# Kernel tuning notes

Measured on AMD Instinct MI355X. Metric: run time of the kernel, lower is better.

Reference implementation:

```python
import jax, jax.numpy as jnp
import numpy as np

B, S, H = 4, 2048, 576
NH, NKV, HD = 9, 3, 64
GROUPS = NH // NKV
ROPE_THETA = 100000.0
MAX_POS = 8192


def _rope_tables():
    inv_freq = 1.0 / (ROPE_THETA ** (jnp.arange(0, HD, 2, dtype=jnp.float32) / HD))
    t = jnp.arange(MAX_POS, dtype=jnp.float32)
    freqs = jnp.outer(t, inv_freq)              # [MAX_POS, HD//2]
    emb = jnp.concatenate([freqs, freqs], axis=-1)  # [MAX_POS, HD]
    return jnp.cos(emb), jnp.sin(emb)


def _rotate_half(x):
    x1, x2 = x[..., : HD // 2], x[..., HD // 2 :]
    return jnp.concatenate([-x2, x1], axis=-1)


def setup_inputs() -> dict:
    key = jax.random.key(0)
    k1, k2, k3, k4, k5 = jax.random.split(key, 5)
    hidden_states = jax.random.normal(k1, (B, S, H), dtype=jnp.float32)
    # causal additive mask [B,1,S,S]: 0 where allowed, large negative above diagonal
    causal = jnp.triu(jnp.ones((S, S), dtype=bool), k=1)
    attention_mask = jnp.where(causal, jnp.float32(-1e9), jnp.float32(0.0))[None, None]
    attention_mask = jnp.broadcast_to(attention_mask, (B, 1, S, S))
    position_ids = jnp.broadcast_to(jnp.arange(S, dtype=jnp.int32)[None, :], (B, S))
    scale = 1.0 / np.sqrt(H)
    Wq = jax.random.normal(k2, (NH * HD, H), dtype=jnp.float32) * scale
    Wk = jax.random.normal(k3, (NKV * HD, H), dtype=jnp.float32) * scale
    Wv = jax.random.normal(k4, (NKV * HD, H), dtype=jnp.float32) * scale
    Wo = jax.random.normal(k5, (H, NH * HD), dtype=jnp.float32) * scale
    return {"hidden_states": hidden_states, "attention_mask": attention_mask,
            "position_ids": position_ids, "Wq": Wq, "Wk": Wk, "Wv": Wv, "Wo": Wo}


def reference(hidden_states, attention_mask, position_ids, Wq, Wk, Wv, Wo):
    bsz, q_len, _ = hidden_states.shape
    cos_cached, sin_cached = _rope_tables()
    # projections (nn.Linear: x @ W.T), reshape to [B, heads, S, HD]
    q = (hidden_states @ Wq.T).reshape(bsz, q_len, NH, HD).transpose(0, 2, 1, 3)
    k = (hidden_states @ Wk.T).reshape(bsz, q_len, NKV, HD).transpose(0, 2, 1, 3)
    v = (hidden_states @ Wv.T).reshape(bsz, q_len, NKV, HD).transpose(0, 2, 1, 3)
    # RoPE: gather cos/sin per position, broadcast over heads
    cos = cos_cached[position_ids][:, None]  # [B,1,S,HD]
    sin = sin_cached[position_ids][:, None]
    q = q * cos + _rotate_half(q) * sin
    k = k * cos + _rotate_half(k) * sin
    # GQA: repeat_interleave kv heads
    k = jnp.repeat(k, GROUPS, axis=1)  # [B,NH,S,HD]
    v = jnp.repeat(v, GROUPS, axis=1)
    scores = jnp.einsum('bhqd,bhkd->bhqk', q, k) / np.sqrt(HD)
    scores = scores + attention_mask
    probs = jax.nn.softmax(scores.astype(jnp.float32), axis=-1).astype(q.dtype)
    attn = jnp.einsum('bhqk,bhkd->bhqd', probs, v)
    attn = attn.transpose(0, 2, 1, 3).reshape(bsz, q_len, NH * HD)
    return attn @ Wo.T
```

## Files before the change

### kernel.cpp

```cpp
#include <hip/hip_runtime.h>
#include <hip/hip_bf16.h>
#include <math.h>

#define Bsz 4
#define Slen 2048
#define Hdim 576
#define NH 9
#define NKV 3
#define HD 64

typedef __bf16 bf16_t;
typedef __bf16 bf16x8 __attribute__((ext_vector_type(8)));
typedef float f32x4 __attribute__((ext_vector_type(4)));
typedef float f32x16 __attribute__((ext_vector_type(16)));
typedef unsigned int u32;
typedef unsigned int u32x4 __attribute__((ext_vector_type(4)));

static __device__ __forceinline__ bf16x8 load_cvt8(const float* __restrict__ src){
  float4 f0 = *reinterpret_cast<const float4*>(src);
  float4 f1 = *reinterpret_cast<const float4*>(src + 4);
  bf16x8 v;
  v[0]=(bf16_t)f0.x; v[1]=(bf16_t)f0.y; v[2]=(bf16_t)f0.z; v[3]=(bf16_t)f0.w;
  v[4]=(bf16_t)f1.x; v[5]=(bf16_t)f1.y; v[6]=(bf16_t)f1.z; v[7]=(bf16_t)f1.w;
  return v;
}

static __device__ __forceinline__ void gload16(const bf16_t* g, bf16_t* l){
  __builtin_amdgcn_global_load_lds((const __attribute__((address_space(1))) void*)g,
                                   (__attribute__((address_space(3))) void*)l, 16, 0, 0);
}

__global__ void setup_kernel(const float* __restrict__ X,
                             const float* __restrict__ Wq,
                             const float* __restrict__ Wk,
                             const float* __restrict__ Wv,
                             const float* __restrict__ Wo,
                             bf16_t* __restrict__ Xb,
                             bf16_t* __restrict__ Wb,
                             bf16_t* __restrict__ Wob,
                             float* __restrict__ cost,
                             float* __restrict__ sint)
{
  const int bid = blockIdx.x;
  if (bid < 256){
    int i = bid * 256 + threadIdx.x;
    int j = i & 31;
    int p = i >> 5;
    double invf = pow(100000.0, -(double)j / 32.0);
    double ang = (double)p * invf;
    cost[i] = (float)cos(ang);
    sint[i] = (float)sin(ang);
    return;
  }
  const int NX  = 8192 * 576 / 8;
  const int NWq = 576 * 576 / 8;
  const int NWk = 192 * 576 / 8;
  int i = (bid - 256) * 256 + threadIdx.x;
  const int total = NX + NWq + 2 * NWk + NWq;
  if (i >= total) return;
  const float* src; bf16_t* dst; int off;
  if (i < NX)                    { src = X;  dst = Xb;            off = i; }
  else if (i < NX + NWq)         { src = Wq; dst = Wb;            off = i - NX; }
  else if (i < NX + NWq + NWk)   { src = Wk; dst = Wb + 331776;   off = i - NX - NWq; }
  else if (i < NX + NWq + 2*NWk) { src = Wv; dst = Wb + 442368;   off = i - NX - NWq - NWk; }
  else                           { src = Wo; dst = Wob;           off = i - NX - NWq - 2*NWk; }
  *reinterpret_cast<bf16x8*>(dst + (size_t)off * 8) = load_cvt8(src + (size_t)off * 8);
}

__launch_bounds__(256)
__global__ void qkv_gemm_kernel(const bf16_t* __restrict__ Xb,
                                const bf16_t* __restrict__ Wb,
                                bf16_t* __restrict__ qbuf,
                                bf16_t* __restrict__ kbuf,
                                bf16_t* __restrict__ vtbuf)
{
  __shared__ bf16_t Ald[2][128 * 64];
  __shared__ bf16_t Bld[2][64 * 64];
  const int t = threadIdx.x, l = t & 63, w = t >> 6;
  const int wm = w >> 1, wn = w & 1;
  const int lane16 = l & 15, grp = l >> 4;
  const int m0 = blockIdx.x * 128;
  const int nt = blockIdx.y;
  const int nrow0 = nt * 64;

  const int sr = l >> 3;
  const int sc = ((l & 7) ^ sr) * 8;

  f32x4 acc[4][2];
  #pragma unroll
  for (int mi = 0; mi < 4; ++mi)
    #pragma unroll
    for (int ni = 0; ni < 2; ++ni)
      acc[mi][ni] = (f32x4){0.f, 0.f, 0.f, 0.f};

  auto STAGE = [&](int kt, int buf){
    const int k0 = kt * 64;
    #pragma unroll
    for (int u = 0; u < 4; ++u)
      gload16(Xb + (size_t)(m0 + w * 32 + u * 8 + sr) * Hdim + k0 + sc,
              &Ald[buf][(w * 32 + u * 8) * 64]);
    #pragma unroll
    for (int u = 0; u < 2; ++u)
      gload16(Wb + (size_t)(nrow0 + w * 16 + u * 8 + sr) * Hdim + k0 + sc,
              &Bld[buf][(w * 16 + u * 8) * 64]);
  };

  STAGE(0, 0);
  asm volatile("s_waitcnt vmcnt(0)" ::: "memory");
  __syncthreads();

  const int sl7 = lane16 & 7;
  for (int kt = 0; kt < 9; ++kt){
    const int buf = kt & 1;
    if (kt + 1 < 9) STAGE(kt + 1, buf ^ 1);
    #pragma unroll
    for (int ks = 0; ks < 2; ++ks){
      bf16x8 a[4], bb[2];
      #pragma unroll
      for (int mi = 0; mi < 4; ++mi){
        int row = wm * 64 + mi * 16 + lane16;
        a[mi] = *reinterpret_cast<const bf16x8*>(&Ald[buf][row * 64 + (((ks * 4 + grp) ^ sl7) * 8)]);
      }
      #pragma unroll
      for (int ni = 0; ni < 2; ++ni){
        int row = wn * 32 + ni * 16 + lane16;
        bb[ni] = *reinterpret_cast<const bf16x8*>(&Bld[buf][row * 64 + (((ks * 4 + grp) ^ sl7) * 8)]);
      }
      #pragma unroll
      for (int mi = 0; mi < 4; ++mi)
        #pragma unroll
        for (int ni = 0; ni < 2; ++ni)
          acc[mi][ni] = __builtin_amdgcn_mfma_f32_16x16x32_bf16(a[mi], bb[ni], acc[mi][ni], 0, 0, 0);
    }
    if (kt + 1 < 9){
      asm volatile("s_waitcnt vmcnt(0)" ::: "memory");
      __syncthreads();
    }
  }

  #pragma unroll
  for (int mi = 0; mi < 4; ++mi){
    #pragma unroll
    for (int ni = 0; ni < 2; ++ni){
      #pragma unroll
      for (int j = 0; j < 4; ++j){
        int m = m0 + wm * 64 + mi * 16 + grp * 4 + j;
        int dl = wn * 32 + ni * 16 + lane16;
        int b = m >> 11;
        int s = m & 2047;
        bf16_t v = (bf16_t)acc[mi][ni][j];
        if (nt < 9)
          qbuf[(((size_t)b * NH + nt) * Slen + s) * HD + dl] = v;
        else if (nt < 12)
          kbuf[(((size_t)b * NKV + (nt - 9)) * Slen + s) * HD + dl] = v;
        else
          vtbuf[(((size_t)b * NKV + (nt - 12)) * HD + dl) * Slen + s] = v;
      }
    }
  }
}

__global__ void rope_apply_all(bf16_t* __restrict__ qkbuf, const int* __restrict__ pos_ids,
                               const float* __restrict__ cost, const float* __restrict__ sint,
                               float qscale)
{
  int idx = blockIdx.x * blockDim.x + threadIdx.x;
  const int qrows = Bsz * NH * Slen;
  const int total = qrows + Bsz * NKV * Slen;
  if (idx >= total) return;
  const bool isq = idx < qrows;
  int s = idx & (Slen - 1);
  int b = isq ? idx / (NH * Slen) : (idx - qrows) / (NKV * Slen);
  float scale = isq ? qscale : 1.0f;
  bf16_t* row = qkbuf + (size_t)idx * HD;
  int pos = pos_ids[b * Slen + s];
  const float* cp = cost + (size_t)pos * 32;
  const float* sp = sint + (size_t)pos * 32;
  float x[64];
  #pragma unroll
  for (int v = 0; v < 8; ++v){
    bf16x8 t8 = *reinterpret_cast<const bf16x8*>(row + v * 8);
    #pragma unroll
    for (int i = 0; i < 8; ++i) x[v * 8 + i] = (float)t8[i];
  }
  bf16_t o[64];
  #pragma unroll
  for (int j = 0; j < 32; ++j){
    float c = cp[j], sn = sp[j];
    o[j]      = (bf16_t)((x[j] * c - x[j + 32] * sn) * scale);
    o[j + 32] = (bf16_t)((x[j + 32] * c + x[j] * sn) * scale);
  }
  #pragma unroll
  for (int v = 0; v < 8; ++v)
    *reinterpret_cast<bf16x8*>(row + v * 8) = *reinterpret_cast<bf16x8*>(o + v * 8);
}

__launch_bounds__(128)
__global__ void flash_attn_kernel(const bf16_t* __restrict__ qbuf,
                                  const bf16_t* __restrict__ kbuf,
                                  const bf16_t* __restrict__ vtbuf,
                                  bf16_t* __restrict__ attn_out,
                                  u32* __restrict__ part_O,
                                  float* __restrict__ part_ml)
{
  __shared__ bf16_t Kld[3][32 * 64];
  __shared__ bf16_t Vld[3][64 * 32];
  const int t = threadIdx.x, l = t & 63, w = t >> 6;
  const int l32 = l & 31, hi = l >> 5;

  const int flat = blockIdx.x;
  const int v = flat / 36;
  const int bh = flat % 36;
  int qt, t0, t1, seg;
  if (v < 16){ qt = 16 + v; t0 = 0; t1 = 32; seg = 0; }
  else {
    int i = (v - 16) >> 1;
    if (((v - 16) & 1) == 0){ qt = 15 - i; t0 = 0; t1 = 2 * qt + 2; seg = -1; }
    else                    { qt = 31 - i; t0 = 32; t1 = 2 * qt + 2; seg = 1; }
  }
  const int b = bh / NH, h = bh % NH, kvh = h / (NH / NKV);

  const bf16_t* qp = qbuf + ((size_t)b * NH + h) * Slen * HD;
  const bf16_t* kp = kbuf + ((size_t)b * NKV + kvh) * Slen * HD;
  const bf16_t* vp = vtbuf + ((size_t)b * NKV + kvh) * HD * Slen;

  const int krow = l >> 3;
  const int ksc  = ((l & 7) ^ krow) * 8;
  const int vrow = l >> 2;
  const int vsc  = ((l & 3) ^ ((vrow >> 1) & 3)) * 8;

  auto STAGE = [&](int kt, int buf){
    const int k0 = kt * 32;
    #pragma unroll
    for (int u = 0; u < 2; ++u){
      int ub = w * 2 + u;
      gload16(kp + (size_t)(k0 + ub * 8 + krow) * HD + ksc, &Kld[buf][ub * 512]);
      gload16(vp + (size_t)(ub * 16 + vrow) * Slen + k0 + vsc, &Vld[buf][ub * 512]);
    }
  };

  STAGE(t0, 0);
  if (t0 + 1 < t1) STAGE(t0 + 1, 1);

  const int q0 = qt * 64 + w * 32;
  bf16x8 aq[4];
  #pragma unroll
  for (int ds = 0; ds < 4; ++ds)
    aq[ds] = *reinterpret_cast<const bf16x8*>(qp + (size_t)(q0 + l32) * HD + ds * 16 + hi * 8);

  f32x16 acco[2];
  #pragma unroll
  for (int db = 0; db < 2; ++db)
    #pragma unroll
    for (int r = 0; r < 16; ++r) acco[db][r] = 0.f;
  float mrun = -1e30f, lrun = 0.f;

  int cur = 0;
  const int dt = 2 * qt + w;
  for (int kb = t0; kb < t1; ++kb){
    if (kb + 1 < t1) asm volatile("s_waitcnt vmcnt(8)" ::: "memory");
    else             asm volatile("s_waitcnt vmcnt(0)" ::: "memory");
    __syncthreads();

    if (kb + 2 < t1){
      int sb = cur + 2; if (sb >= 3) sb -= 3;
      STAGE(kb + 2, sb);
    }

    if (kb <= dt){
      f32x16 sacc;
      #pragma unroll
      for (int r = 0; r < 16; ++r) sacc[r] = 0.f;
      __builtin_amdgcn_s_setprio(1);
      #pragma unroll
      for (int ds = 0; ds < 4; ++ds){
        bf16x8 ak = *reinterpret_cast<const bf16x8*>(
            &Kld[cur][l32 * 64 + (((ds * 2 + hi) ^ (l32 & 7)) * 8)]);
        sacc = __builtin_amdgcn_mfma_f32_32x32x16_bf16(ak, aq[ds], sacc, 0, 0, 0);
      }
      __builtin_amdgcn_s_setprio(0);

      if (kb == dt){
        #pragma unroll
        for (int r = 0; r < 16; ++r){
          int crow = (r & 3) + 8 * (r >> 2) + 4 * hi;
          if (crow > l32) sacc[r] = -1e30f;
        }
      }

      float tmax = fmaxf(sacc[0], sacc[1]);
      #pragma unroll
      for (int r = 2; r < 16; ++r) tmax = fmaxf(tmax, sacc[r]);
      tmax = fmaxf(tmax, __shfl_xor(tmax, 32, 64));

      if (__ballot(tmax - mrun > 8.f)){
        float mnew = fmaxf(mrun, tmax);
        float sf = __builtin_amdgcn_exp2f(mrun - mnew);
        lrun *= sf;
        #pragma unroll
        for (int db = 0; db < 2; ++db)
          #pragma unroll
          for (int r = 0; r < 16; ++r) acco[db][r] *= sf;
        mrun = mnew;
      }

      float rsum = 0.f;
      #pragma unroll
      for (int r = 0; r < 16; ++r){
        float pv = __builtin_amdgcn_exp2f(sacc[r] - mrun);
        sacc[r] = pv;
        rsum += pv;
      }
      rsum += __shfl_xor(rsum, 32, 64);
      lrun += rsum;

      u32 wv[8];
      #pragma unroll
      for (int j = 0; j < 8; ++j){
        float lo = sacc[2 * j], hp = sacc[2 * j + 1];
        asm("v_cvt_pk_bf16_f32 %0, %1, %2" : "=v"(wv[j]) : "v"(lo), "v"(hp));
      }
      asm volatile("v_permlane32_swap_b32 %0, %1" : "+v"(wv[0]), "+v"(wv[2]));
      asm volatile("v_permlane32_swap_b32 %0, %1" : "+v"(wv[1]), "+v"(wv[3]));
      asm volatile("v_permlane32_swap_b32 %0, %1" : "+v"(wv[4]), "+v"(wv[6]));
      asm volatile("v_permlane32_swap_b32 %0, %1" : "+v"(wv[5]), "+v"(wv[7]));
      u32x4 pa0 = (u32x4){wv[0], wv[1], wv[2], wv[3]};
      u32x4 pa1 = (u32x4){wv[4], wv[5], wv[6], wv[7]};

      __builtin_amdgcn_s_setprio(1);
      #pragma unroll
      for (int ks = 0; ks < 2; ++ks){
        #pragma unroll
        for (int db = 0; db < 2; ++db){
          bf16x8 av = *reinterpret_cast<const bf16x8*>(
              &Vld[cur][(db * 32 + l32) * 32 + (((ks * 2 + hi) ^ ((l32 >> 1) & 3)) * 8)]);
          acco[db] = __builtin_amdgcn_mfma_f32_32x32x16_bf16(
              av, __builtin_bit_cast(bf16x8, ks ? pa1 : pa0), acco[db], 0, 0, 0);
        }
      }
      __builtin_amdgcn_s_setprio(0);
    }

    cur = (cur + 1 == 3) ? 0 : cur + 1;
  }

  if (seg < 0){
    const float linv = 1.0f / lrun;
    const int srow = q0 + l32;
    bf16_t* orow = attn_out + ((size_t)b * Slen + srow) * (NH * HD) + h * HD;
    #pragma unroll
    for (int db = 0; db < 2; ++db){
      #pragma unroll
      for (int j = 0; j < 8; ++j){
        int r = 2 * j;
        int d = db * 32 + (r & 3) + 8 * (r >> 2) + 4 * hi;
        u32 pw;
        float lo = acco[db][r] * linv, hp = acco[db][r + 1] * linv;
        asm("v_cvt_pk_bf16_f32 %0, %1, %2" : "=v"(pw) : "v"(lo), "v"(hp));
        *reinterpret_cast<u32*>(orow + d) = pw;
      }
    }
  } else {
    const int slot = (bh * 16 + (qt - 16)) * 2 + seg;
    u32* po = part_O + ((size_t)slot * 2 + w) * 1024;
    float* pml = part_ml + ((size_t)slot * 2 + w) * 64;
    #pragma unroll
    for (int db = 0; db < 2; ++db){
      #pragma unroll
      for (int j = 0; j < 8; ++j){
        int r = 2 * j;
        int d = db * 32 + (r & 3) + 8 * (r >> 2) + 4 * hi;
        u32 pw;
        float lo = acco[db][r], hp = acco[db][r + 1];
        asm("v_cvt_pk_bf16_f32 %0, %1, %2" : "=v"(pw) : "v"(lo), "v"(hp));
        po[(d >> 1) * 32 + l32] = pw;
      }
    }
    if (hi == 0){ pml[l32] = mrun; pml[32 + l32] = lrun; }
  }
}

__launch_bounds__(128)
__global__ void combine_kernel(const u32* __restrict__ part_O,
                               const float* __restrict__ part_ml,
                               bf16_t* __restrict__ attn_out)
{
  const int idx = blockIdx.x;
  const int bh = idx % 36, qtm = idx / 36;
  const int qt = 16 + qtm;
  const int b = bh / NH, h = bh % NH;
  const int t = threadIdx.x;
  const int q = t & 31, wg = (t >> 5) & 1, half = t >> 6;
  const int slot0 = (bh * 16 + qtm) * 2;

  const float* pml0 = part_ml + ((size_t)(slot0 + 0) * 2 + wg) * 64;
  const float* pml1 = part_ml + ((size_t)(slot0 + 1) * 2 + wg) * 64;
  float m1 = pml0[q], l1 = pml0[32 + q];
  float m2 = pml1[q], l2 = pml1[32 + q];
  float m = fmaxf(m1, m2);
  float a1 = __builtin_amdgcn_exp2f(m1 - m);
  float a2 = __builtin_amdgcn_exp2f(m2 - m);
  float linv = 1.0f / (l1 * a1 + l2 * a2);
  a1 *= linv; a2 *= linv;

  const u32* po0 = part_O + ((size_t)(slot0 + 0) * 2 + wg) * 1024;
  const u32* po1 = part_O + ((size_t)(slot0 + 1) * 2 + wg) * 1024;
  const int s = qt * 64 + wg * 32 + q;
  bf16_t* orow = attn_out + ((size_t)b * Slen + s) * (NH * HD) + h * HD;

  #pragma unroll
  for (int u = 0; u < 16; ++u){
    int dp = half * 16 + u;
    u32 v1 = po0[dp * 32 + q], v2 = po1[dp * 32 + q];
    float lo = a1 * __builtin_bit_cast(float, v1 << 16)
             + a2 * __builtin_bit_cast(float, v2 << 16);
    float hv = a1 * __builtin_bit_cast(float, v1 & 0xffff0000u)
             + a2 * __builtin_bit_cast(float, v2 & 0xffff0000u);
    u32 pw;
    asm("v_cvt_pk_bf16_f32 %0, %1, %2" : "=v"(pw) : "v"(lo), "v"(hv));
    *reinterpret_cast<u32*>(orow + 2 * dp) = pw;
  }
}

__launch_bounds__(256)
__global__ void out_gemm_kernel(const bf16_t* __restrict__ A,
                                const bf16_t* __restrict__ Wob,
                                float* __restrict__ out)
{
  __shared__ bf16_t Ald[2][128 * 64];
  __shared__ bf16_t Bld[2][64 * 64];
  const int t = threadIdx.x, l = t & 63, w = t >> 6;
  const int wm = w >> 1, wn = w & 1;
  const int lane16 = l & 15, grp = l >> 4;
  const int m0 = blockIdx.x * 128;
  const int nt = blockIdx.y;
  const int nrow0 = nt * 64;

  const int sr = l >> 3;
  const int sc = ((l & 7) ^ sr) * 8;

  f32x4 acc[4][2];
  #pragma unroll
  for (int mi = 0; mi < 4; ++mi)
    #pragma unroll
    for (int ni = 0; ni < 2; ++ni)
      acc[mi][ni] = (f32x4){0.f, 0.f, 0.f, 0.f};

  auto STAGE = [&](int kt, int buf){
    const int k0 = kt * 64;
    #pragma unroll
    for (int u = 0; u < 4; ++u)
      gload16(A + (size_t)(m0 + w * 32 + u * 8 + sr) * Hdim + k0 + sc,
              &Ald[buf][(w * 32 + u * 8) * 64]);
    #pragma unroll
    for (int u = 0; u < 2; ++u)
      gload16(Wob + (size_t)(nrow0 + w * 16 + u * 8 + sr) * Hdim + k0 + sc,
              &Bld[buf][(w * 16 + u * 8) * 64]);
  };

  STAGE(0, 0);
  asm volatile("s_waitcnt vmcnt(0)" ::: "memory");
  __syncthreads();

  const int sl7 = lane16 & 7;
  for (int kt = 0; kt < 9; ++kt){
    const int buf = kt & 1;
    if (kt + 1 < 9) STAGE(kt + 1, buf ^ 1);
    #pragma unroll
    for (int ks = 0; ks < 2; ++ks){
      bf16x8 a[4], bb[2];
      #pragma unroll
      for (int mi = 0; mi < 4; ++mi){
        int row = wm * 64 + mi * 16 + lane16;
        a[mi] = *reinterpret_cast<const bf16x8*>(&Ald[buf][row * 64 + (((ks * 4 + grp) ^ sl7) * 8)]);
      }
      #pragma unroll
      for (int ni = 0; ni < 2; ++ni){
        int row = wn * 32 + ni * 16 + lane16;
        bb[ni] = *reinterpret_cast<const bf16x8*>(&Bld[buf][row * 64 + (((ks * 4 + grp) ^ sl7) * 8)]);
      }
      #pragma unroll
      for (int mi = 0; mi < 4; ++mi)
        #pragma unroll
        for (int ni = 0; ni < 2; ++ni)
          acc[mi][ni] = __builtin_amdgcn_mfma_f32_16x16x32_bf16(a[mi], bb[ni], acc[mi][ni], 0, 0, 0);
    }
    if (kt + 1 < 9){
      asm volatile("s_waitcnt vmcnt(0)" ::: "memory");
      __syncthreads();
    }
  }

  #pragma unroll
  for (int mi = 0; mi < 4; ++mi){
    #pragma unroll
    for (int ni = 0; ni < 2; ++ni){
      #pragma unroll
      for (int j = 0; j < 4; ++j){
        int m = m0 + wm * 64 + mi * 16 + grp * 4 + j;
        int n = nrow0 + wn * 32 + ni * 16 + lane16;
        out[(size_t)m * Hdim + n] = acc[mi][ni][j];
      }
    }
  }
}

extern "C" void kernel_launch(void* const* d_in, const int* in_sizes, int n_in,
                              void* d_out, int out_size, void* d_ws, size_t ws_size,
                              hipStream_t stream) {
  const float* X   = (const float*)d_in[0];
  const int* pos   = (const int*)d_in[2];
  const float* Wq  = (const float*)d_in[3];
  const float* Wk  = (const float*)d_in[4];
  const float* Wv  = (const float*)d_in[5];
  const float* Wo  = (const float*)d_in[6];
  float* out = (float*)d_out;

  char* ws = (char*)d_ws;
  float* cost = (float*)ws;
  float* sint = (float*)(ws + 262144);
  bf16_t* qb  = (bf16_t*)(ws + 524288);
  bf16_t* kb  = qb + (size_t)Bsz * NH * Slen * HD;
  bf16_t* vt  = kb + (size_t)Bsz * NKV * Slen * HD;
  bf16_t* Xb  = vt + (size_t)Bsz * NKV * Slen * HD;
  bf16_t* ab  = Xb;
  bf16_t* Wb  = Xb + (size_t)8192 * 576;
  bf16_t* Wob = Wb + (size_t)960 * 576;
  u32*  part_O  = (u32*)(Wob + (size_t)576 * 576);
  float* part_ml = (float*)(part_O + (size_t)1152 * 2 * 1024);

  const float QSCALE = 0.125f * 1.44269504088896f;

  setup_kernel<<<dim3(256 + 2736), dim3(256), 0, stream>>>(X, Wq, Wk, Wv, Wo, Xb, Wb, Wob, cost, sint);
  qkv_gemm_kernel<<<dim3(64, 15), dim3(256), 0, stream>>>(Xb, Wb, qb, kb, vt);
  rope_apply_all<<<dim3((Bsz * (NH + NKV) * Slen + 255) / 256), dim3(256), 0, stream>>>(qb, pos, cost, sint, QSCALE);
  flash_attn_kernel<<<dim3(1728), dim3(128), 0, stream>>>(qb, kb, vt, ab, part_O, part_ml);
  combine_kernel<<<dim3(576), dim3(128), 0, stream>>>(part_O, part_ml, ab);
  out_gemm_kernel<<<dim3(64, 9), dim3(256), 0, stream>>>(ab, Wob, out);
}
```

Before: 113.5 us.

## Split K/V load waits so QK^T and softmax overlap the V tile load

Each stage now issues its K loads before its V loads, and the loop waits in two steps. It first waits only for the K tile, computes scores and softmax, then waits for V behind a second barrier before the PV MFMAs. This lets the V tile keep arriving during QK^T and softmax. The Q register load is moved ahead of the staging loads, and the max and sum reductions become trees to shorten the dependency chains. It adds an extra __syncthreads per iteration, and the hand-coded vmcnt values must exactly match the number of loads in flight.

After: 119.1 us. 5.0% more time.

```diff
diff --git a/kernel.cpp b/kernel.cpp
--- a/kernel.cpp
+++ b/kernel.cpp
@@ -28,6 +28,13 @@
 static __device__ __forceinline__ void gload16(const bf16_t* g, bf16_t* l){
   __builtin_amdgcn_global_load_lds((const __attribute__((address_space(1))) void*)g,
                                    (__attribute__((address_space(3))) void*)l, 16, 0, 0);
+}
+
+static __device__ __forceinline__ float xhalf_max(float x){
+  return fmaxf(x, __shfl_xor(x, 32, 64));
+}
+static __device__ __forceinline__ float xhalf_sum(float x){
+  return x + __shfl_xor(x, 32, 64);
 }
 
 __global__ void setup_kernel(const float* __restrict__ X,
@@ -235,18 +242,22 @@
     for (int u = 0; u < 2; ++u){
       int ub = w * 2 + u;
       gload16(kp + (size_t)(k0 + ub * 8 + krow) * HD + ksc, &Kld[buf][ub * 512]);
+    }
+    #pragma unroll
+    for (int u = 0; u < 2; ++u){
+      int ub = w * 2 + u;
       gload16(vp + (size_t)(ub * 16 + vrow) * Slen + k0 + vsc, &Vld[buf][ub * 512]);
     }
   };
+
+  const int q0 = qt * 64 + w * 32;
+  bf16x8 aq[4];
+  #pragma unroll
+  for (int ds = 0; ds < 4; ++ds)
+    aq[ds] = *reinterpret_cast<const bf16x8*>(qp + (size_t)(q0 + l32) * HD + ds * 16 + hi * 8);
 
   STAGE(t0, 0);
   if (t0 + 1 < t1) STAGE(t0 + 1, 1);
-
-  const int q0 = qt * 64 + w * 32;
-  bf16x8 aq[4];
-  #pragma unroll
-  for (int ds = 0; ds < 4; ++ds)
-    aq[ds] = *reinterpret_cast<const bf16x8*>(qp + (size_t)(q0 + l32) * HD + ds * 16 + hi * 8);
 
   f32x16 acco[2];
   #pragma unroll
@@ -258,17 +269,19 @@
   int cur = 0;
   const int dt = 2 * qt + w;
   for (int kb = t0; kb < t1; ++kb){
-    if (kb + 1 < t1) asm volatile("s_waitcnt vmcnt(8)" ::: "memory");
-    else             asm volatile("s_waitcnt vmcnt(0)" ::: "memory");
+    const bool rem1 = (kb + 1 < t1), rem2 = (kb + 2 < t1);
+
+    if (rem1) asm volatile("s_waitcnt vmcnt(6)" ::: "memory");
+    else      asm volatile("s_waitcnt vmcnt(2)" ::: "memory");
     __syncthreads();
 
-    if (kb + 2 < t1){
+    if (rem2){
       int sb = cur + 2; if (sb >= 3) sb -= 3;
       STAGE(kb + 2, sb);
     }
 
+    f32x16 sacc;
     if (kb <= dt){
-      f32x16 sacc;
       #pragma unroll
       for (int r = 0; r < 16; ++r) sacc[r] = 0.f;
       __builtin_amdgcn_s_setprio(1);
@@ -288,10 +301,13 @@
         }
       }
 
-      float tmax = fmaxf(sacc[0], sacc[1]);
-      #pragma unroll
-      for (int r = 2; r < 16; ++r) tmax = fmaxf(tmax, sacc[r]);
-      tmax = fmaxf(tmax, __shfl_xor(tmax, 32, 64));
+      float m0_ = fmaxf(sacc[0], sacc[1]),  m1_ = fmaxf(sacc[2], sacc[3]);
+      float m2_ = fmaxf(sacc[4], sacc[5]),  m3_ = fmaxf(sacc[6], sacc[7]);
+      float m4_ = fmaxf(sacc[8], sacc[9]),  m5_ = fmaxf(sacc[10], sacc[11]);
+      float m6_ = fmaxf(sacc[12], sacc[13]), m7_ = fmaxf(sacc[14], sacc[15]);
+      m0_ = fmaxf(m0_, m1_); m2_ = fmaxf(m2_, m3_); m4_ = fmaxf(m4_, m5_); m6_ = fmaxf(m6_, m7_);
+      float tmax = fmaxf(fmaxf(m0_, m2_), fmaxf(m4_, m6_));
+      tmax = xhalf_max(tmax);
 
       if (__ballot(tmax - mrun > 8.f)){
         float mnew = fmaxf(mrun, tmax);
@@ -304,16 +320,20 @@
         mrun = mnew;
       }
 
-      float rsum = 0.f;
-      #pragma unroll
-      for (int r = 0; r < 16; ++r){
-        float pv = __builtin_amdgcn_exp2f(sacc[r] - mrun);
-        sacc[r] = pv;
-        rsum += pv;
-      }
-      rsum += __shfl_xor(rsum, 32, 64);
-      lrun += rsum;
-
+      #pragma unroll
+      for (int r = 0; r < 16; ++r)
+        sacc[r] = __builtin_amdgcn_exp2f(sacc[r] - mrun);
+      float s0 = sacc[0] + sacc[1],  s1 = sacc[2] + sacc[3];
+      float s2 = sacc[4] + sacc[5],  s3 = sacc[6] + sacc[7];
+      float s4 = sacc[8] + sacc[9],  s5 = sacc[10] + sacc[11];
+      float s6 = sacc[12] + sacc[13], s7 = sacc[14] + sacc[15];
+      s0 += s1; s2 += s3; s4 += s5; s6 += s7;
+      float rsum = (s0 + s2) + (s4 + s6);
+      lrun += xhalf_sum(rsum);
+    }
+
+    u32x4 pa0, pa1;
+    if (kb <= dt){
       u32 wv[8];
       #pragma unroll
       for (int j = 0; j < 8; ++j){
@@ -324,9 +344,16 @@
       asm volatile("v_permlane32_swap_b32 %0, %1" : "+v"(wv[1]), "+v"(wv[3]));
       asm volatile("v_permlane32_swap_b32 %0, %1" : "+v"(wv[4]), "+v"(wv[6]));
       asm volatile("v_permlane32_swap_b32 %0, %1" : "+v"(wv[5]), "+v"(wv[7]));
-      u32x4 pa0 = (u32x4){wv[0], wv[1], wv[2], wv[3]};
-      u32x4 pa1 = (u32x4){wv[4], wv[5], wv[6], wv[7]};
-
+      pa0 = (u32x4){wv[0], wv[1], wv[2], wv[3]};
+      pa1 = (u32x4){wv[4], wv[5], wv[6], wv[7]};
+    }
+
+    if (rem2)      asm volatile("s_waitcnt vmcnt(8)" ::: "memory");
+    else if (rem1) asm volatile("s_waitcnt vmcnt(4)" ::: "memory");
+    else           asm volatile("s_waitcnt vmcnt(0)" ::: "memory");
+    __syncthreads();
+
+    if (kb <= dt){
       __builtin_amdgcn_s_setprio(1);
       #pragma unroll
       for (int ks = 0; ks < 2; ++ks){
```
